# Kernel optimization log

Measured on AMD Instinct MI355X. Metric: run time of the kernel, lower is better.

The kernel has to match this reference:

```python
import itertools
import jax, jax.numpy as jnp
import numpy as np

B, S, H = 1, 2048, 1024
NH, KVH, HD = 16, 8, 64
E, TOPK, I = 8, 2, 3584
EPS = 1e-6
THETA = 1000000.0
COMBS = np.array(list(itertools.combinations(range(E), TOPK)), dtype=np.int32)  # [28,2]


def setup_inputs() -> dict:
    key = jax.random.key(0)
    ks = jax.random.split(key, 12)
    s = 0.02
    return {
        "hidden_states": jax.random.normal(ks[0], (B, S, H), jnp.float32),
        "ln1_w": jnp.ones((H,), jnp.float32),
        "ln2_w": jnp.ones((H,), jnp.float32),
        "wq": jax.random.normal(ks[1], (NH * HD, H), jnp.float32) * s,
        "wk": jax.random.normal(ks[2], (KVH * HD, H), jnp.float32) * s,
        "wv": jax.random.normal(ks[3], (KVH * HD, H), jnp.float32) * s,
        "wo": jax.random.normal(ks[4], (H, NH * HD), jnp.float32) * s,
        "gate_w": jax.random.normal(ks[5], (E, H), jnp.float32) * s,
        "w1": jax.random.normal(ks[6], (E, I, H), jnp.float32) * s,
        "w2": jax.random.normal(ks[7], (E, H, I), jnp.float32) * s,
        "w3": jax.random.normal(ks[8], (E, I, H), jnp.float32) * s,
    }


def _rmsnorm(x, w):
    v = x.astype(jnp.float32)
    v = v * jax.lax.rsqrt(jnp.mean(v * v, axis=-1, keepdims=True) + EPS)
    return (w * v).astype(x.dtype)


def _rotate_half(x):
    h = x.shape[-1] // 2
    return jnp.concatenate([-x[..., h:], x[..., :h]], axis=-1)


def reference(hidden_states, ln1_w, ln2_w, wq, wk, wv, wo, gate_w, w1, w2, w3):
    residual = hidden_states
    x = _rmsnorm(hidden_states, ln1_w)

    # --- Mixtral attention (GQA + RoPE, causal) ---
    q = (x @ wq.T).reshape(B, S, NH, HD).transpose(0, 2, 1, 3)   # [B,NH,S,HD]
    k = (x @ wk.T).reshape(B, S, KVH, HD).transpose(0, 2, 1, 3)  # [B,KVH,S,HD]
    v = (x @ wv.T).reshape(B, S, KVH, HD).transpose(0, 2, 1, 3)

    pos = jnp.arange(S, dtype=jnp.float32)
    inv_freq = 1.0 / (THETA ** (jnp.arange(0, HD, 2, dtype=jnp.float32) / HD))
    freqs = pos[:, None] * inv_freq[None, :]               # [S,HD/2]
    emb = jnp.concatenate([freqs, freqs], axis=-1)          # [S,HD]
    cos, sin = jnp.cos(emb)[None, None], jnp.sin(emb)[None, None]
    q = q * cos + _rotate_half(q) * sin
    k = k * cos + _rotate_half(k) * sin

    rep = NH // KVH
    k = jnp.repeat(k, rep, axis=1)
    v = jnp.repeat(v, rep, axis=1)

    scores = jnp.einsum("bhsd,bhtd->bhst", q, k) / jnp.sqrt(jnp.float32(HD))
    causal = jnp.tril(jnp.ones((S, S), dtype=bool))
    scores = jnp.where(causal[None, None], scores, jnp.finfo(jnp.float32).min)
    attn = jax.nn.softmax(scores.astype(jnp.float32), axis=-1).astype(q.dtype)
    ctx = jnp.einsum("bhst,bhtd->bhsd", attn, v)
    ctx = ctx.transpose(0, 2, 1, 3).reshape(B, S, NH * HD)
    hidden_states = residual + ctx @ wo.T

    # --- MoE block (combination routing, no experts_used mask) ---
    residual = hidden_states
    x = _rmsnorm(hidden_states, ln2_w).reshape(-1, H)       # [N,H], N=B*S
    N = x.shape[0]
    router_logits = x @ gate_w.T                            # [N,E]
    rw = jax.nn.softmax(router_logits.astype(jnp.float32), axis=-1)

    combs = jnp.asarray(COMBS)                              # [28,2]
    comb_scores = jnp.take(rw, combs, axis=1).sum(-1)       # [N,28]
    sel = jnp.argmax(comb_scores, axis=-1)                  # [N]
    selected_experts = combs[sel]                           # [N,TOPK]
    w = jnp.take_along_axis(rw, selected_experts, axis=1)   # [N,TOPK]
    w = (w / w.sum(-1, keepdims=True)).astype(x.dtype)

    # per-token per-expert combine weights (0 if not selected)
    wm = jnp.zeros((N, E), x.dtype).at[jnp.arange(N)[:, None], selected_experts].set(w)

    # dense evaluation of all experts, combined by sparse weights
    h1 = jax.nn.silu(jnp.einsum("nh,eih->nei", x, w1))
    h3 = jnp.einsum("nh,eih->nei", x, w3)
    out_e = jnp.einsum("nei,ehi->neh", h1 * h3, w2)          # [N,E,H]
    moe_out = jnp.einsum("neh,ne->nh", out_e, wm)

    hidden_states = residual + moe_out.reshape(B, S, H)
    return hidden_states
```

## Files before the change

### kernel.cpp

```cpp
#include <hip/hip_runtime.h>
#include <hip/hip_bf16.h>
#include <math.h>

constexpr int S_ = 2048, H_ = 1024, NH_ = 16, KVH_ = 8, HD_ = 64;
constexpr int E_ = 8, I_ = 3584;
constexpr int KSLC = 4;
constexpr float EPS_ = 1e-6f;
constexpr float THETA_ = 1000000.0f;

#define SDIV(a,b) (((a)+(b)-1)/(b))

typedef __attribute__((ext_vector_type(8))) short bf16x8;
typedef __attribute__((ext_vector_type(4))) float f32x4;

__device__ inline unsigned pkbf(float a, float b) {
    unsigned r;
    asm("v_cvt_pk_bf16_f32 %0, %1, %2" : "=v"(r) : "v"(a), "v"(b));
    return r;
}
__device__ inline unsigned short f2bf(float f) {
    unsigned u = __float_as_uint(f);
    u += 0x7FFF + ((u >> 16) & 1);
    return (unsigned short)(u >> 16);
}
__device__ inline float bf2f(unsigned short v) {
    return __uint_as_float((unsigned)v << 16);
}

__device__ inline void gload16u(const void* gsrc, char* ldsArr, int uoff) {
    int off = __builtin_amdgcn_readfirstlane(uoff);
    __builtin_amdgcn_global_load_lds(
        (__attribute__((address_space(1))) void*)(gsrc),
        (__attribute__((address_space(3))) void*)(ldsArr + off), 16, 0, 0);
}
__device__ inline void vmdrain() {
    asm volatile("s_waitcnt vmcnt(0)" ::: "memory");
}

template<bool WB>
__device__ inline int4 loadW16(const void* W, size_t elemOff) {
    if constexpr (WB) {
        return *(const int4*)((const unsigned short*)W + elemOff);
    } else {
        const float* s = (const float*)W + elemOff;
        float4 f0 = *(const float4*)s, f1 = *(const float4*)(s + 4);
        return make_int4(pkbf(f0.x, f0.y), pkbf(f0.z, f0.w),
                         pkbf(f1.x, f1.y), pkbf(f1.z, f1.w));
    }
}

__global__ __launch_bounds__(256) void conv_bf16(const float* __restrict__ in,
                                                 unsigned short* __restrict__ out, long n8)
{
    long i = (long)blockIdx.x * 256 + threadIdx.x;
    long stride = (long)gridDim.x * 256;
    for (; i < n8; i += stride) {
        const float* s = in + i * 8;
        float4 f0 = *(const float4*)s, f1 = *(const float4*)(s + 4);
        *(int4*)(out + i * 8) = make_int4(pkbf(f0.x, f0.y), pkbf(f0.z, f0.w),
                                          pkbf(f1.x, f1.y), pkbf(f1.z, f1.w));
    }
}

__global__ __launch_bounds__(256) void rmsnorm_k(const float* __restrict__ x,
                                                 const float* __restrict__ w,
                                                 float* __restrict__ out,
                                                 unsigned short* __restrict__ outb)
{
    int row = blockIdx.x;
    int tid = threadIdx.x;
    const float* xr = x + (size_t)row * H_;
    float4 v = *(const float4*)&xr[tid * 4];
    float ss = v.x*v.x + v.y*v.y + v.z*v.z + v.w*v.w;
#pragma unroll
    for (int off = 32; off > 0; off >>= 1) ss += __shfl_xor(ss, off);
    __shared__ float red[4];
    if ((tid & 63) == 0) red[tid >> 6] = ss;
    __syncthreads();
    float tot = red[0] + red[1] + red[2] + red[3];
    float r = rsqrtf(tot / (float)H_ + EPS_);
    float4 wv = *(const float4*)&w[tid * 4];
    float4 o;
    o.x = v.x * r * wv.x; o.y = v.y * r * wv.y;
    o.z = v.z * r * wv.z; o.w = v.w * r * wv.w;
    *(float4*)&out[(size_t)row * H_ + tid * 4] = o;
    if (outb) {
        uint2 pk = make_uint2(pkbf(o.x, o.y), pkbf(o.z, o.w));
        *(uint2*)&outb[(size_t)row * H_ + tid * 4] = pk;
    }
}

template<bool OUTF32>
__global__ __launch_bounds__(256) void dense_g(const unsigned short* __restrict__ A,
                                               const unsigned short* __restrict__ B,
                                               const float* __restrict__ Res,
                                               void* __restrict__ C,
                                               int K, int ldC)
{
    int m0 = blockIdx.y * 128, n0 = blockIdx.x * 64;
    int tid = threadIdx.x;
    __shared__ char As[16384], Bs[8192];
    int lane = tid & 63, w = tid >> 6, wm = w >> 1, wn = w & 1;
    int lm = lane & 15, lk = lane >> 4;
    int wb16 = (tid & ~63) * 16;

    const unsigned short* aSrc[4];
    const unsigned short* bSrc[2];
#pragma unroll
    for (int it = 0; it < 4; ++it) {
        int g = tid + it * 256, row = g >> 3, kg = g & 7;
        int kgs = kg ^ (row & 7);
        aSrc[it] = A + (size_t)(m0 + row) * K + kgs * 8;
    }
#pragma unroll
    for (int it = 0; it < 2; ++it) {
        int g = tid + it * 256, row = g >> 3, kg = g & 7;
        int kgs = kg ^ (row & 7);
        bSrc[it] = B + (size_t)(n0 + row) * K + kgs * 8;
    }

    f32x4 z = {0.f, 0.f, 0.f, 0.f};
    f32x4 acc[4][2];
#pragma unroll
    for (int mf = 0; mf < 4; ++mf)
#pragma unroll
        for (int nf = 0; nf < 2; ++nf) acc[mf][nf] = z;

    for (int kt = 0; kt < K / 64; ++kt) {
        int kb = kt * 64;
#pragma unroll
        for (int it = 0; it < 4; ++it)
            gload16u(aSrc[it] + kb, As, wb16 + it * 4096);
#pragma unroll
        for (int it = 0; it < 2; ++it)
            gload16u(bSrc[it] + kb, Bs, wb16 + it * 4096);
        vmdrain();
        __syncthreads();
#pragma unroll
        for (int ks = 0; ks < 2; ++ks) {
            bf16x8 af[4];
#pragma unroll
            for (int mf = 0; mf < 4; ++mf) {
                int row = wm * 64 + mf * 16 + lm;
                af[mf] = *(const bf16x8*)(As + row * 128 + ((ks * 64 + lk * 16) ^ ((row & 7) << 4)));
            }
#pragma unroll
            for (int nf = 0; nf < 2; ++nf) {
                int brow = wn * 32 + nf * 16 + lm;
                bf16x8 bf = *(const bf16x8*)(Bs + brow * 128 + ((ks * 64 + lk * 16) ^ ((brow & 7) << 4)));
#pragma unroll
                for (int mf = 0; mf < 4; ++mf)
                    acc[mf][nf] = __builtin_amdgcn_mfma_f32_16x16x32_bf16(af[mf], bf, acc[mf][nf], 0, 0, 0);
            }
        }
        __syncthreads();
    }

#pragma unroll
    for (int mf = 0; mf < 4; ++mf)
#pragma unroll
        for (int nf = 0; nf < 2; ++nf) {
            int col = n0 + wn * 32 + nf * 16 + lm;
#pragma unroll
            for (int j = 0; j < 4; ++j) {
                int row = m0 + wm * 64 + mf * 16 + lk * 4 + j;
                float v = acc[mf][nf][j];
                if constexpr (OUTF32) {
                    float r = Res ? Res[(size_t)row * ldC + col] : 0.0f;
                    ((float*)C)[(size_t)row * ldC + col] = v + r;
                } else {
                    ((unsigned short*)C)[(size_t)row * ldC + col] = f2bf(v);
                }
            }
        }
}

template<bool WB>
__global__ __launch_bounds__(256) void dense_mfma(const float* __restrict__ A,
                                                  const void* __restrict__ Bw,
                                                  const float* __restrict__ Res,
                                                  float* __restrict__ C,
                                                  int M, int N, int K)
{
    __shared__ char As[16384], Bs[16384];
    int tid = threadIdx.x;
    int m0 = blockIdx.y * 128, n0 = blockIdx.x * 128;
    int lane = tid & 63, w = tid >> 6, wm = w >> 1, wn = w & 1;
    int lm = lane & 15, lk = lane >> 4;

    int4 rA[4], rB[4];
    auto loadAll = [&](int kb) {
#pragma unroll
        for (int it = 0; it < 4; ++it) {
            int g = tid + it * 256, row = g >> 3, kg = g & 7;
            const float* s = A + (size_t)(m0 + row) * K + kb + kg * 8;
            float4 f0 = *(const float4*)s, f1 = *(const float4*)(s + 4);
            rA[it] = make_int4(pkbf(f0.x, f0.y), pkbf(f0.z, f0.w),
                               pkbf(f1.x, f1.y), pkbf(f1.z, f1.w));
            rB[it] = loadW16<WB>(Bw, (size_t)(n0 + row) * K + kb + kg * 8);
        }
    };
    auto writeAll = [&]() {
#pragma unroll
        for (int it = 0; it < 4; ++it) {
            int g = tid + it * 256, row = g >> 3, kg = g & 7;
            int byte = row * 128 + ((kg * 16) ^ ((row & 7) << 4));
            *(int4*)(As + byte) = rA[it];
            *(int4*)(Bs + byte) = rB[it];
        }
    };

    f32x4 z = {0.f, 0.f, 0.f, 0.f};
    f32x4 acc[4][4];
#pragma unroll
    for (int mf = 0; mf < 4; ++mf)
#pragma unroll
        for (int nf = 0; nf < 4; ++nf) acc[mf][nf] = z;

    loadAll(0);
    for (int kt = 0; kt < K / 64; ++kt) {
        __syncthreads();
        writeAll();
        __syncthreads();
        if (kt + 1 < K / 64) loadAll((kt + 1) * 64);
#pragma unroll
        for (int ks = 0; ks < 2; ++ks) {
            bf16x8 af[4];
#pragma unroll
            for (int mf = 0; mf < 4; ++mf) {
                int row = wm * 64 + mf * 16 + lm;
                af[mf] = *(const bf16x8*)(As + row * 128 + ((ks * 64 + lk * 16) ^ ((row & 7) << 4)));
            }
#pragma unroll
            for (int nf = 0; nf < 4; ++nf) {
                int brow = wn * 64 + nf * 16 + lm;
                bf16x8 bf = *(const bf16x8*)(Bs + brow * 128 + ((ks * 64 + lk * 16) ^ ((brow & 7) << 4)));
#pragma unroll
                for (int mf = 0; mf < 4; ++mf)
                    acc[mf][nf] = __builtin_amdgcn_mfma_f32_16x16x32_bf16(af[mf], bf, acc[mf][nf], 0, 0, 0);
            }
        }
    }

#pragma unroll
    for (int mf = 0; mf < 4; ++mf)
#pragma unroll
        for (int nf = 0; nf < 4; ++nf) {
            int col = n0 + wn * 64 + nf * 16 + lm;
#pragma unroll
            for (int j = 0; j < 4; ++j) {
                int row = m0 + wm * 64 + mf * 16 + lk * 4 + j;
                float r = Res ? Res[(size_t)row * N + col] : 0.0f;
                C[(size_t)row * N + col] = acc[mf][nf][j] + r;
            }
        }
}

__global__ __launch_bounds__(256) void rope_conv_b(const unsigned short* __restrict__ qkvb,
                                                   unsigned short* __restrict__ qbf,
                                                   unsigned short* __restrict__ kbf)
{
    int idx = blockIdx.x * 256 + threadIdx.x;
    const int totq = S_ * NH_ * 32;
    const int tot = totq + S_ * KVH_ * 32;
    if (idx >= tot) return;
    const unsigned short* src; unsigned short* dst; int s, di; float sc;
    if (idx < totq) {
        s = idx / (NH_ * 32); int r = idx % (NH_ * 32); int h = r >> 5;
        src = qkvb + (size_t)s * 2048 + h * 64;
        dst = qbf + ((size_t)s * NH_ + h) * HD_;
        di = r & 31; sc = 0.125f;
    } else {
        int j2 = idx - totq;
        s = j2 / (KVH_ * 32); int r = j2 % (KVH_ * 32); int kvh = r >> 5;
        src = qkvb + (size_t)s * 2048 + 1024 + kvh * 64;
        dst = kbf + ((size_t)s * KVH_ + kvh) * HD_;
        di = r & 31; sc = 1.0f;
    }
    float invf = powf(THETA_, -(2.0f * di) / (float)HD_);
    float ang = (float)s * invf;
    float c = cosf(ang), sn = sinf(ang);
    float x0 = bf2f(src[di]), x1 = bf2f(src[di + 32]);
    dst[di]      = f2bf((x0 * c - x1 * sn) * sc);
    dst[di + 32] = f2bf((x1 * c + x0 * sn) * sc);
}

__global__ __launch_bounds__(256) void v_trans_b(const unsigned short* __restrict__ qkvb,
                                                 unsigned short* __restrict__ vtb)
{
    int t0 = blockIdx.x * 64, kvh = blockIdx.y;
    __shared__ unsigned short T[64][64];
    int tid = threadIdx.x;
    int k = tid >> 2, d0 = (tid & 3) * 16;
    const unsigned short* src = qkvb + (size_t)(t0 + k) * 2048 + 1536 + kvh * 64 + d0;
    *(int4*)&T[k][d0]     = *(const int4*)(src);
    *(int4*)&T[k][d0 + 8] = *(const int4*)(src + 8);
    __syncthreads();
    int d = tid >> 2, s0 = (tid & 3) * 16;
    unsigned short tmp[16] __attribute__((aligned(16)));
#pragma unroll
    for (int x = 0; x < 16; ++x) {
        int s = s0 + x;
        int key = 16 * (s & 3) + (s >> 2);
        tmp[x] = T[key][d];
    }
    unsigned short* dst = vtb + ((size_t)kvh * HD_ + d) * S_ + t0 + s0;
    *(int4*)(dst)     = *(int4*)(tmp);
    *(int4*)(dst + 8) = *(int4*)(tmp + 8);
}

__global__ __launch_bounds__(256) void rope_conv(const float* __restrict__ q,
                                                 const float* __restrict__ k,
                                                 unsigned short* __restrict__ qbf,
                                                 unsigned short* __restrict__ kbf)
{
    int idx = blockIdx.x * 256 + threadIdx.x;
    const int totq = S_ * NH_ * 32;
    const int tot = totq + S_ * KVH_ * 32;
    if (idx >= tot) return;
    const float* base; unsigned short* obase; int s, di; float sc;
    if (idx < totq) {
        s = idx / (NH_ * 32); int r = idx % (NH_ * 32);
        size_t o = ((size_t)s * NH_ + (r >> 5)) * HD_;
        base = q + o; obase = qbf + o; di = r & 31; sc = 0.125f;
    } else {
        int j2 = idx - totq;
        s = j2 / (KVH_ * 32); int r = j2 % (KVH_ * 32);
        size_t o = ((size_t)s * KVH_ + (r >> 5)) * HD_;
        base = k + o; obase = kbf + o; di = r & 31; sc = 1.0f;
    }
    float invf = powf(THETA_, -(2.0f * di) / (float)HD_);
    float ang = (float)s * invf;
    float c = cosf(ang), sn = sinf(ang);
    float x0 = base[di], x1 = base[di + 32];
    obase[di]      = f2bf((x0 * c - x1 * sn) * sc);
    obase[di + 32] = f2bf((x1 * c + x0 * sn) * sc);
}

__global__ __launch_bounds__(256) void v_trans(const float* __restrict__ v,
                                               unsigned short* __restrict__ vtb)
{
    int t0 = blockIdx.x * 64, kvh = blockIdx.y;
    __shared__ unsigned short T[64][64];
    int tid = threadIdx.x;
    int k = tid >> 2, d0 = (tid & 3) * 16;
    const float* src = v + ((size_t)(t0 + k) * KVH_ + kvh) * HD_ + d0;
#pragma unroll
    for (int x = 0; x < 4; ++x) {
        float4 f = *(const float4*)(src + x * 4);
        T[k][d0 + x*4 + 0] = f2bf(f.x);
        T[k][d0 + x*4 + 1] = f2bf(f.y);
        T[k][d0 + x*4 + 2] = f2bf(f.z);
        T[k][d0 + x*4 + 3] = f2bf(f.w);
    }
    __syncthreads();
    int d = tid >> 2, s0 = (tid & 3) * 16;
    unsigned short tmp[16] __attribute__((aligned(16)));
#pragma unroll
    for (int x = 0; x < 16; ++x) {
        int s = s0 + x;
        int key = 16 * (s & 3) + (s >> 2);
        tmp[x] = T[key][d];
    }
    unsigned short* dst = vtb + ((size_t)kvh * HD_ + d) * S_ + t0 + s0;
    *(int4*)(dst)     = *(int4*)(tmp);
    *(int4*)(dst + 8) = *(int4*)(tmp + 8);
}

__global__ __launch_bounds__(256) void attn_mfma(const unsigned short* __restrict__ qbf,
                                                 const unsigned short* __restrict__ kbf,
                                                 const unsigned short* __restrict__ vtb,
                                                 float* __restrict__ ctx,
                                                 unsigned short* __restrict__ ctxb)
{
    __shared__ char Ps[4 * 2048];
    int pair = blockIdx.x, h = blockIdx.y, z = blockIdx.z;
    int qb = z ? (31 - pair) : pair;
    int q0 = qb * 64;
    int kvh = h >> 1;
    int tid = threadIdx.x;
    int w = tid >> 6, lane = tid & 63;
    int lm = lane & 15, lk = lane >> 4;
    char* myP = Ps + w * 2048;

    bf16x8 qf[2];
    const unsigned short* qrow = qbf + ((size_t)(q0 + w * 16 + lm) * NH_ + h) * HD_;
#pragma unroll
    for (int ks = 0; ks < 2; ++ks)
        qf[ks] = *(const bf16x8*)(qrow + ks * 32 + lk * 8);

    float m_[4], l_[4];
    f32x4 o_[4];
#pragma unroll
    for (int j = 0; j < 4; ++j) { m_[j] = -1e30f; l_[j] = 0.f; }
    f32x4 zf = {0.f, 0.f, 0.f, 0.f};
#pragma unroll
    for (int nd = 0; nd < 4; ++nd) o_[nd] = zf;

    for (int t0 = 0; t0 <= q0; t0 += 64) {
        f32x4 s[4];
#pragma unroll
        for (int nf = 0; nf < 4; ++nf) {
            const unsigned short* krow = kbf + ((size_t)(t0 + nf * 16 + lm) * KVH_ + kvh) * HD_;
            bf16x8 k0 = *(const bf16x8*)(krow + lk * 8);
            bf16x8 k1 = *(const bf16x8*)(krow + 32 + lk * 8);
            f32x4 acc = zf;
            acc = __builtin_amdgcn_mfma_f32_16x16x32_bf16(qf[0], k0, acc, 0, 0, 0);
            acc = __builtin_amdgcn_mfma_f32_16x16x32_bf16(qf[1], k1, acc, 0, 0, 0);
            s[nf] = acc;
        }
        if (t0 == q0) {
#pragma unroll
            for (int nf = 0; nf < 4; ++nf)
#pragma unroll
                for (int j = 0; j < 4; ++j) {
                    int key = nf * 16 + lm, qq = w * 16 + lk * 4 + j;
                    if (key > qq) s[nf][j] = -1e30f;
                }
        }
        float p_[4][4];
#pragma unroll
        for (int j = 0; j < 4; ++j) {
            float mx = fmaxf(fmaxf(s[0][j], s[1][j]), fmaxf(s[2][j], s[3][j]));
#pragma unroll
            for (int off = 8; off > 0; off >>= 1) mx = fmaxf(mx, __shfl_xor(mx, off));
            float nm = fmaxf(m_[j], mx);
            float rs = __expf(m_[j] - nm);
            float sum = 0.f;
#pragma unroll
            for (int nf = 0; nf < 4; ++nf) {
                float pv = __expf(s[nf][j] - nm);
                p_[nf][j] = pv; sum += pv;
            }
#pragma unroll
            for (int off = 8; off > 0; off >>= 1) sum += __shfl_xor(sum, off);
            l_[j] = l_[j] * rs + sum;
            m_[j] = nm;
#pragma unroll
            for (int nd = 0; nd < 4; ++nd) o_[nd][j] *= rs;
        }
#pragma unroll
        for (int j = 0; j < 4; ++j) {
            int r = lk * 4 + j;
            unsigned lo = pkbf(p_[0][j], p_[1][j]);
            unsigned hi = pkbf(p_[2][j], p_[3][j]);
            int byte = (lm * 8) ^ ((r & 7) << 4);
            *(uint2*)(myP + r * 128 + byte) = make_uint2(lo, hi);
        }
#pragma unroll
        for (int ks = 0; ks < 2; ++ks) {
            int byte = (ks * 64 + lk * 16) ^ ((lm & 7) << 4);
            bf16x8 pA = *(const bf16x8*)(myP + lm * 128 + byte);
#pragma unroll
            for (int nd = 0; nd < 4; ++nd) {
                const unsigned short* vrow = vtb + ((size_t)kvh * HD_ + nd * 16 + lm) * S_ + t0 + ks * 32 + lk * 8;
                bf16x8 vB = *(const bf16x8*)vrow;
                o_[nd] = __builtin_amdgcn_mfma_f32_16x16x32_bf16(pA, vB, o_[nd], 0, 0, 0);
            }
        }
    }
#pragma unroll
    for (int nd = 0; nd < 4; ++nd)
#pragma unroll
        for (int j = 0; j < 4; ++j) {
            int r = lk * 4 + j;
            float val = o_[nd][j] / l_[j];
            size_t oidx = ((size_t)(q0 + w * 16 + r) * NH_ + h) * HD_ + nd * 16 + lm;
            ctx[oidx] = val;
            ctxb[oidx] = f2bf(val);
        }
}

__global__ __launch_bounds__(64) void router_k(const float* __restrict__ x2,
                                               const float* __restrict__ gw,
                                               int* __restrict__ cnt,
                                               int* __restrict__ elist,
                                               int* __restrict__ eslot,
                                               float* __restrict__ wslot)
{
    int n = blockIdx.x, lane = threadIdx.x;
    float part[E_];
#pragma unroll
    for (int e = 0; e < E_; ++e) part[e] = 0.f;
    const float* xr = x2 + (size_t)n * H_;
    for (int j = lane; j < H_; j += 64) {
        float xv = xr[j];
#pragma unroll
        for (int e = 0; e < E_; ++e) part[e] = fmaf(xv, gw[e * H_ + j], part[e]);
    }
#pragma unroll
    for (int e = 0; e < E_; ++e)
#pragma unroll
        for (int off = 32; off > 0; off >>= 1) part[e] += __shfl_xor(part[e], off);
    if (lane == 0) {
        float mx = part[0];
#pragma unroll
        for (int e = 1; e < E_; ++e) mx = fmaxf(mx, part[e]);
        float rw[E_]; float ssum = 0.f;
#pragma unroll
        for (int e = 0; e < E_; ++e) { rw[e] = expf(part[e] - mx); ssum += rw[e]; }
#pragma unroll
        for (int e = 0; e < E_; ++e) rw[e] /= ssum;
        float best = -1.f; int ba = 0, bb = 1;
        for (int a = 0; a < E_; ++a)
            for (int b = a + 1; b < E_; ++b) {
                float scv = rw[a] + rw[b];
                if (scv > best) { best = scv; ba = a; bb = b; }
            }
        float wa = rw[ba], wb = rw[bb], wsum = wa + wb;
        wa /= wsum; wb /= wsum;
        int p = atomicAdd(&cnt[ba], 1);
        elist[ba * S_ + p] = n; eslot[ba * S_ + p] = 2 * n;
        p = atomicAdd(&cnt[bb], 1);
        elist[bb * S_ + p] = n; eslot[bb * S_ + p] = 2 * n + 1;
        wslot[2 * n] = wa; wslot[2 * n + 1] = wb;
    }
}

__global__ __launch_bounds__(256) void moe_up_g(const unsigned short* __restrict__ x2b,
                                                const unsigned short* __restrict__ w1b,
                                                const unsigned short* __restrict__ w3b,
                                                const int* __restrict__ cnt,
                                                const int* __restrict__ elist,
                                                const int* __restrict__ eslot,
                                                unsigned short* __restrict__ hbuf)
{
    int e = blockIdx.z;
    int c = cnt[e];
    int p0 = blockIdx.y * 128;
    if (p0 >= c) return;
    int i0 = blockIdx.x * 64;
    int tid = threadIdx.x;

    __shared__ char As[16384], B1s[8192], B3s[8192];
    __shared__ int rowtokS[128], rowslotS[128];
    if (tid < 128) {
        int p = min(p0 + tid, c - 1);
        rowtokS[tid]  = elist[e * S_ + p];
        rowslotS[tid] = eslot[e * S_ + p];
    }
    __syncthreads();

    int lane = tid & 63, w = tid >> 6, wm = w >> 1, wn = w & 1;
    int lm = lane & 15, lk = lane >> 4;
    int wb16 = (tid & ~63) * 16;
    size_t wbase = (size_t)e * I_ * H_;

    const unsigned short* aSrc[4];
    const unsigned short* b1Src[2];
    const unsigned short* b3Src[2];
#pragma unroll
    for (int it = 0; it < 4; ++it) {
        int g = tid + it * 256, row = g >> 3, kg = g & 7;
        int kgs = kg ^ (row & 7);
        aSrc[it] = x2b + (size_t)rowtokS[row] * H_ + kgs * 8;
    }
#pragma unroll
    for (int it = 0; it < 2; ++it) {
        int g = tid + it * 256, row = g >> 3, kg = g & 7;
        int kgs = kg ^ (row & 7);
        size_t off = wbase + (size_t)(i0 + row) * H_ + kgs * 8;
        b1Src[it] = w1b + off;
        b3Src[it] = w3b + off;
    }

    f32x4 z = {0.f, 0.f, 0.f, 0.f};
    f32x4 acc1[4][2], acc3[4][2];
#pragma unroll
    for (int mf = 0; mf < 4; ++mf)
#pragma unroll
        for (int nf = 0; nf < 2; ++nf) { acc1[mf][nf] = z; acc3[mf][nf] = z; }

    for (int kt = 0; kt < H_ / 64; ++kt) {
        int kb = kt * 64;
#pragma unroll
        for (int it = 0; it < 4; ++it)
            gload16u(aSrc[it] + kb, As, wb16 + it * 4096);
#pragma unroll
        for (int it = 0; it < 2; ++it) {
            gload16u(b1Src[it] + kb, B1s, wb16 + it * 4096);
            gload16u(b3Src[it] + kb, B3s, wb16 + it * 4096);
        }
        vmdrain();
        __syncthreads();
#pragma unroll
        for (int ks = 0; ks < 2; ++ks) {
            bf16x8 af[4];
#pragma unroll
            for (int mf = 0; mf < 4; ++mf) {
                int row = wm * 64 + mf * 16 + lm;
                af[mf] = *(const bf16x8*)(As + row * 128 + ((ks * 64 + lk * 16) ^ ((row & 7) << 4)));
            }
#pragma unroll
            for (int nf = 0; nf < 2; ++nf) {
                int brow = wn * 32 + nf * 16 + lm;
                int bby = brow * 128 + ((ks * 64 + lk * 16) ^ ((brow & 7) << 4));
                bf16x8 b1 = *(const bf16x8*)(B1s + bby);
                bf16x8 b3 = *(const bf16x8*)(B3s + bby);
#pragma unroll
                for (int mf = 0; mf < 4; ++mf) {
                    acc1[mf][nf] = __builtin_amdgcn_mfma_f32_16x16x32_bf16(af[mf], b1, acc1[mf][nf], 0, 0, 0);
                    acc3[mf][nf] = __builtin_amdgcn_mfma_f32_16x16x32_bf16(af[mf], b3, acc3[mf][nf], 0, 0, 0);
                }
            }
        }
        __syncthreads();
    }

#pragma unroll
    for (int mf = 0; mf < 4; ++mf)
#pragma unroll
        for (int nf = 0; nf < 2; ++nf) {
            int coli = i0 + wn * 32 + nf * 16 + lm;
#pragma unroll
            for (int j = 0; j < 4; ++j) {
                int rloc = wm * 64 + mf * 16 + lk * 4 + j;
                if (p0 + rloc < c) {
                    float h1 = acc1[mf][nf][j];
                    float val = h1 / (1.f + __expf(-h1)) * acc3[mf][nf][j];
                    hbuf[(size_t)rowslotS[rloc] * I_ + coli] = f2bf(val);
                }
            }
        }
}

__global__ __launch_bounds__(256) void moe_dn_g(const unsigned short* __restrict__ hbuf,
                                                const unsigned short* __restrict__ w2b,
                                                const int* __restrict__ cnt,
                                                const int* __restrict__ eslot,
                                                unsigned short* __restrict__ dbuf)
{
    int e = blockIdx.z >> 2;
    int slice = blockIdx.z & 3;
    int c = cnt[e];
    int p0 = blockIdx.y * 128;
    if (p0 >= c) return;
    int h0 = blockIdx.x * 128;
    int tid = threadIdx.x;
    const int kb0 = slice * (I_ / KSLC);

    __shared__ char As[16384], Bs[16384];
    __shared__ int rowslotS[128];
    if (tid < 128) rowslotS[tid] = eslot[e * S_ + min(p0 + tid, c - 1)];
    __syncthreads();

    int lane = tid & 63, w = tid >> 6, wm = w >> 1, wn = w & 1;
    int lm = lane & 15, lk = lane >> 4;
    int wb16 = (tid & ~63) * 16;
    size_t wbase = (size_t)e * H_ * I_;

    const unsigned short* aSrc[4];
    const unsigned short* bSrc[4];
#pragma unroll
    for (int it = 0; it < 4; ++it) {
        int g = tid + it * 256, row = g >> 3, kg = g & 7;
        int kgs = kg ^ (row & 7);
        aSrc[it] = hbuf + (size_t)rowslotS[row] * I_ + kb0 + kgs * 8;
        bSrc[it] = w2b + wbase + (size_t)(h0 + row) * I_ + kb0 + kgs * 8;
    }

    f32x4 z = {0.f, 0.f, 0.f, 0.f};
    f32x4 acc[4][4];
#pragma unroll
    for (int mf = 0; mf < 4; ++mf)
#pragma unroll
        for (int nf = 0; nf < 4; ++nf) acc[mf][nf] = z;

    const int NKT = (I_ / KSLC) / 64;
    for (int kt = 0; kt < NKT; ++kt) {
        int kb = kt * 64;
#pragma unroll
        for (int it = 0; it < 4; ++it) {
            gload16u(aSrc[it] + kb, As, wb16 + it * 4096);
            gload16u(bSrc[it] + kb, Bs, wb16 + it * 4096);
        }
        vmdrain();
        __syncthreads();
#pragma unroll
        for (int ks = 0; ks < 2; ++ks) {
            bf16x8 af[4];
#pragma unroll
            for (int mf = 0; mf < 4; ++mf) {
                int row = wm * 64 + mf * 16 + lm;
                af[mf] = *(const bf16x8*)(As + row * 128 + ((ks * 64 + lk * 16) ^ ((row & 7) << 4)));
            }
#pragma unroll
            for (int nf = 0; nf < 4; ++nf) {
                int brow = wn * 64 + nf * 16 + lm;
                bf16x8 bf = *(const bf16x8*)(Bs + brow * 128 + ((ks * 64 + lk * 16) ^ ((brow & 7) << 4)));
#pragma unroll
                for (int mf = 0; mf < 4; ++mf)
                    acc[mf][nf] = __builtin_amdgcn_mfma_f32_16x16x32_bf16(af[mf], bf, acc[mf][nf], 0, 0, 0);
            }
        }
        __syncthreads();
    }

    unsigned short* dslice = dbuf + (size_t)slice * S_ * 2 * H_;
#pragma unroll
    for (int mf = 0; mf < 4; ++mf)
#pragma unroll
        for (int nf = 0; nf < 4; ++nf) {
            int colh = h0 + wn * 64 + nf * 16 + lm;
#pragma unroll
            for (int j = 0; j < 4; ++j) {
                int rloc = wm * 64 + mf * 16 + lk * 4 + j;
                if (p0 + rloc < c)
                    dslice[(size_t)rowslotS[rloc] * H_ + colh] = f2bf(acc[mf][nf][j]);
            }
        }
}

template<bool WB>
__global__ __launch_bounds__(256) void moe_up_mfma(const float* __restrict__ x2,
                                                   const void* __restrict__ w1,
                                                   const void* __restrict__ w3,
                                                   const int* __restrict__ cnt,
                                                   const int* __restrict__ elist,
                                                   const int* __restrict__ eslot,
                                                   unsigned short* __restrict__ hbuf)
{
    int e = blockIdx.z;
    int c = cnt[e];
    int p0 = blockIdx.y * 128;
    if (p0 >= c) return;
    int i0 = blockIdx.x * 64;
    int tid = threadIdx.x;

    __shared__ char As[16384], B1s[8192], B3s[8192];
    __shared__ int rowtokS[128], rowslotS[128];
    if (tid < 128) {
        int p = min(p0 + tid, c - 1);
        rowtokS[tid]  = elist[e * S_ + p];
        rowslotS[tid] = eslot[e * S_ + p];
    }
    __syncthreads();

    int lane = tid & 63, w = tid >> 6, wm = w >> 1, wn = w & 1;
    int lm = lane & 15, lk = lane >> 4;
    size_t wbase = (size_t)e * I_ * H_;

    int4 rA[4], rB1[2], rB3[2];
    auto loadAll = [&](int kb) {
#pragma unroll
        for (int it = 0; it < 4; ++it) {
            int g = tid + it * 256, row = g >> 3, kg = g & 7;
            const float* s = x2 + (size_t)rowtokS[row] * H_ + kb + kg * 8;
            float4 f0 = *(const float4*)s, f1 = *(const float4*)(s + 4);
            rA[it] = make_int4(pkbf(f0.x, f0.y), pkbf(f0.z, f0.w),
                               pkbf(f1.x, f1.y), pkbf(f1.z, f1.w));
        }
#pragma unroll
        for (int it = 0; it < 2; ++it) {
            int g = tid + it * 256, row = g >> 3, kg = g & 7;
            size_t off = wbase + (size_t)(i0 + row) * H_ + kb + kg * 8;
            rB1[it] = loadW16<WB>(w1, off);
            rB3[it] = loadW16<WB>(w3, off);
        }
    };
    auto writeAll = [&]() {
#pragma unroll
        for (int it = 0; it < 4; ++it) {
            int g = tid + it * 256, row = g >> 3, kg = g & 7;
            int byte = row * 128 + ((kg * 16) ^ ((row & 7) << 4));
            *(int4*)(As + byte) = rA[it];
        }
#pragma unroll
        for (int it = 0; it < 2; ++it) {
            int g = tid + it * 256, row = g >> 3, kg = g & 7;
            int byte = row * 128 + ((kg * 16) ^ ((row & 7) << 4));
            *(int4*)(B1s + byte) = rB1[it];
            *(int4*)(B3s + byte) = rB3[it];
        }
    };

    f32x4 z = {0.f, 0.f, 0.f, 0.f};
    f32x4 acc1[4][2], acc3[4][2];
#pragma unroll
    for (int mf = 0; mf < 4; ++mf)
#pragma unroll
        for (int nf = 0; nf < 2; ++nf) { acc1[mf][nf] = z; acc3[mf][nf] = z; }

    loadAll(0);
    for (int kt = 0; kt < H_ / 64; ++kt) {
        __syncthreads();
        writeAll();
        __syncthreads();
        if (kt + 1 < H_ / 64) loadAll((kt + 1) * 64);
#pragma unroll
        for (int ks = 0; ks < 2; ++ks) {
            bf16x8 af[4];
#pragma unroll
            for (int mf = 0; mf < 4; ++mf) {
                int row = wm * 64 + mf * 16 + lm;
                af[mf] = *(const bf16x8*)(As + row * 128 + ((ks * 64 + lk * 16) ^ ((row & 7) << 4)));
            }
#pragma unroll
            for (int nf = 0; nf < 2; ++nf) {
                int brow = wn * 32 + nf * 16 + lm;
                int bby = brow * 128 + ((ks * 64 + lk * 16) ^ ((brow & 7) << 4));
                bf16x8 b1 = *(const bf16x8*)(B1s + bby);
                bf16x8 b3 = *(const bf16x8*)(B3s + bby);
#pragma unroll
                for (int mf = 0; mf < 4; ++mf) {
                    acc1[mf][nf] = __builtin_amdgcn_mfma_f32_16x16x32_bf16(af[mf], b1, acc1[mf][nf], 0, 0, 0);
                    acc3[mf][nf] = __builtin_amdgcn_mfma_f32_16x16x32_bf16(af[mf], b3, acc3[mf][nf], 0, 0, 0);
                }
            }
        }
    }

#pragma unroll
    for (int mf = 0; mf < 4; ++mf)
#pragma unroll
        for (int nf = 0; nf < 2; ++nf) {
            int coli = i0 + wn * 32 + nf * 16 + lm;
#pragma unroll
            for (int j = 0; j < 4; ++j) {
                int rloc = wm * 64 + mf * 16 + lk * 4 + j;
                if (p0 + rloc < c) {
                    float h1 = acc1[mf][nf][j];
                    float val = h1 / (1.f + __expf(-h1)) * acc3[mf][nf][j];
                    hbuf[(size_t)rowslotS[rloc] * I_ + coli] = f2bf(val);
                }
            }
        }
}

template<bool WB>
__global__ __launch_bounds__(256) void moe_dn_mfma(const unsigned short* __restrict__ hbuf,
                                                   const void* __restrict__ w2,
                                                   const int* __restrict__ cnt,
                                                   const int* __restrict__ eslot,
                                                   unsigned short* __restrict__ dbuf)
{
    int e = blockIdx.z >> 2;
    int slice = blockIdx.z & 3;
    int c = cnt[e];
    int p0 = blockIdx.y * 128;
    if (p0 >= c) return;
    int h0 = blockIdx.x * 128;
    int tid = threadIdx.x;
    const int kb0 = slice * (I_ / KSLC);

    __shared__ char As[16384], Bs[16384];
    __shared__ int rowslotS[128];
    if (tid < 128) rowslotS[tid] = eslot[e * S_ + min(p0 + tid, c - 1)];
    __syncthreads();

    int lane = tid & 63, w = tid >> 6, wm = w >> 1, wn = w & 1;
    int lm = lane & 15, lk = lane >> 4;
    size_t wbase = (size_t)e * H_ * I_;

    int4 rA[4], rB[4];
    auto loadAll = [&](int kb) {
#pragma unroll
        for (int it = 0; it < 4; ++it) {
            int g = tid + it * 256, row = g >> 3, kg = g & 7;
            rA[it] = *(const int4*)(hbuf + (size_t)rowslotS[row] * I_ + kb + kg * 8);
            rB[it] = loadW16<WB>(w2, wbase + (size_t)(h0 + row) * I_ + kb + kg * 8);
        }
    };
    auto writeAll = [&]() {
#pragma unroll
        for (int it = 0; it < 4; ++it) {
            int g = tid + it * 256, row = g >> 3, kg = g & 7;
            int byte = row * 128 + ((kg * 16) ^ ((row & 7) << 4));
            *(int4*)(As + byte) = rA[it];
            *(int4*)(Bs + byte) = rB[it];
        }
    };

    f32x4 z = {0.f, 0.f, 0.f, 0.f};
    f32x4 acc[4][4];
#pragma unroll
    for (int mf = 0; mf < 4; ++mf)
#pragma unroll
        for (int nf = 0; nf < 4; ++nf) acc[mf][nf] = z;

    loadAll(kb0);
    const int NKT = (I_ / KSLC) / 64;
    for (int kt = 0; kt < NKT; ++kt) {
        __syncthreads();
        writeAll();
        __syncthreads();
        if (kt + 1 < NKT) loadAll(kb0 + (kt + 1) * 64);
#pragma unroll
        for (int ks = 0; ks < 2; ++ks) {
            bf16x8 af[4];
#pragma unroll
            for (int mf = 0; mf < 4; ++mf) {
                int row = wm * 64 + mf * 16 + lm;
                af[mf] = *(const bf16x8*)(As + row * 128 + ((ks * 64 + lk * 16) ^ ((row & 7) << 4)));
            }
#pragma unroll
            for (int nf = 0; nf < 4; ++nf) {
                int brow = wn * 64 + nf * 16 + lm;
                bf16x8 bf = *(const bf16x8*)(Bs + brow * 128 + ((ks * 64 + lk * 16) ^ ((brow & 7) << 4)));
#pragma unroll
                for (int mf = 0; mf < 4; ++mf)
                    acc[mf][nf] = __builtin_amdgcn_mfma_f32_16x16x32_bf16(af[mf], bf, acc[mf][nf], 0, 0, 0);
            }
        }
    }

    unsigned short* dslice = dbuf + (size_t)slice * S_ * 2 * H_;
#pragma unroll
    for (int mf = 0; mf < 4; ++mf)
#pragma unroll
        for (int nf = 0; nf < 4; ++nf) {
            int colh = h0 + wn * 64 + nf * 16 + lm;
#pragma unroll
            for (int j = 0; j < 4; ++j) {
                int rloc = wm * 64 + mf * 16 + lk * 4 + j;
                if (p0 + rloc < c)
                    dslice[(size_t)rowslotS[rloc] * H_ + colh] = f2bf(acc[mf][nf][j]);
            }
        }
}

__global__ __launch_bounds__(256) void combine_k(const float* __restrict__ hid2,
                                                 const unsigned short* __restrict__ dbuf,
                                                 const float* __restrict__ wslot,
                                                 float* __restrict__ out)
{
    int idx = blockIdx.x * 256 + threadIdx.x;
    if (idx >= S_ * H_) return;
    int n = idx >> 10;
    int hcol = idx & (H_ - 1);
    float s0 = 0.f, s1 = 0.f;
#pragma unroll
    for (int sl = 0; sl < KSLC; ++sl) {
        const unsigned short* base = dbuf + (size_t)sl * S_ * 2 * H_;
        s0 += bf2f(base[(size_t)(2 * n)     * H_ + hcol]);
        s1 += bf2f(base[(size_t)(2 * n + 1) * H_ + hcol]);
    }
    out[idx] = hid2[idx] + wslot[2 * n] * s0 + wslot[2 * n + 1] * s1;
}

extern "C" void kernel_launch(void* const* d_in, const int* in_sizes, int n_in,
                              void* d_out, int out_size, void* d_ws, size_t ws_size,
                              hipStream_t stream)
{
    const float* hidden = (const float*)d_in[0];
    const float* ln1    = (const float*)d_in[1];
    const float* ln2    = (const float*)d_in[2];
    const float* wq     = (const float*)d_in[3];
    const float* wk     = (const float*)d_in[4];
    const float* wv     = (const float*)d_in[5];
    const float* wo     = (const float*)d_in[6];
    const float* gw     = (const float*)d_in[7];
    const float* w1     = (const float*)d_in[8];
    const float* w2     = (const float*)d_in[9];
    const float* w3     = (const float*)d_in[10];
    float* out = (float*)d_out;

    char* p = (char*)d_ws;
    auto alignp = [&]() { p = (char*)(((uintptr_t)p + 255) & ~(uintptr_t)255); };
    auto alloc_f = [&](size_t n) { alignp(); float* r = (float*)p; p += n * 4; return r; };
    auto alloc_h = [&](size_t n) { alignp(); unsigned short* r = (unsigned short*)p; p += n * 2; return r; };
    auto alloc_i = [&](size_t n) { alignp(); int* r = (int*)p; p += n * 4; return r; };

    float* xb   = alloc_f((size_t)S_ * H_);
    unsigned short* xbb = alloc_h((size_t)S_ * H_);
    float* q    = alloc_f((size_t)S_ * NH_ * HD_);
    float* kb   = alloc_f((size_t)S_ * KVH_ * HD_);
    float* vb   = alloc_f((size_t)S_ * KVH_ * HD_);
    unsigned short* qkvb = alloc_h((size_t)S_ * 2048);
    float* hid2 = alloc_f((size_t)S_ * H_);
    float* x2   = alloc_f((size_t)S_ * H_);
    unsigned short* x2b  = alloc_h((size_t)S_ * H_);
    unsigned short* ctxb = alloc_h((size_t)S_ * H_);
    unsigned short* hbuf = alloc_h((size_t)S_ * 2 * I_);
    unsigned short* dbuf = alloc_h((size_t)KSLC * S_ * 2 * H_);
    float* wslot= alloc_f((size_t)S_ * 2);
    unsigned short* qbf = alloc_h((size_t)S_ * NH_ * HD_);
    unsigned short* kbf = alloc_h((size_t)S_ * KVH_ * HD_);
    unsigned short* vtb = alloc_h((size_t)KVH_ * HD_ * S_);
    int* cnt   = alloc_i(E_);
    int* elist = alloc_i((size_t)E_ * S_);
    int* eslot = alloc_i((size_t)E_ * S_);
    float* ctx = xb;

    size_t used = (size_t)(p - (char*)d_ws);
    const size_t nW = (size_t)E_ * I_ * H_;
    size_t wbf_bytes = (3 * nW + (size_t)2048 * H_ + (size_t)H_ * NH_ * HD_) * 2 + 8192;
    bool WB = ws_size > used && (ws_size - used) >= wbf_bytes;

    unsigned short *w1b = nullptr, *w3b = nullptr, *w2b = nullptr;
    unsigned short *wqkvb = nullptr, *wob = nullptr;
    if (WB) {
        w1b = alloc_h(nW); w3b = alloc_h(nW); w2b = alloc_h(nW);
        wqkvb = alloc_h((size_t)2048 * H_);
        wob = alloc_h((size_t)H_ * NH_ * HD_);
    }

    hipMemsetAsync(cnt, 0, E_ * sizeof(int), stream);

    if (WB) {
        conv_bf16<<<2048, 256, 0, stream>>>(w1, w1b, (long)(nW / 8));
        conv_bf16<<<2048, 256, 0, stream>>>(w3, w3b, (long)(nW / 8));
        conv_bf16<<<2048, 256, 0, stream>>>(w2, w2b, (long)(nW / 8));
        conv_bf16<<<512, 256, 0, stream>>>(wq, wqkvb, (long)((size_t)NH_*HD_*H_ / 8));
        conv_bf16<<<256, 256, 0, stream>>>(wk, wqkvb + (size_t)NH_*HD_*H_, (long)((size_t)KVH_*HD_*H_ / 8));
        conv_bf16<<<256, 256, 0, stream>>>(wv, wqkvb + (size_t)(NH_+KVH_)*HD_*H_, (long)((size_t)KVH_*HD_*H_ / 8));
        conv_bf16<<<512, 256, 0, stream>>>(wo, wob, (long)((size_t)H_*NH_*HD_ / 8));
    }

    rmsnorm_k<<<S_, 256, 0, stream>>>(hidden, ln1, xb, WB ? xbb : nullptr);

    if (WB) {
        dense_g<false><<<dim3(32, 16), 256, 0, stream>>>(xbb, wqkvb, nullptr, qkvb, H_, 2048);
        {
            int tot = S_ * (NH_ + KVH_) * 32;
            rope_conv_b<<<SDIV(tot, 256), 256, 0, stream>>>(qkvb, qbf, kbf);
        }
        v_trans_b<<<dim3(S_ / 64, KVH_), 256, 0, stream>>>(qkvb, vtb);
        attn_mfma<<<dim3(16, NH_, 2), 256, 0, stream>>>(qbf, kbf, vtb, ctx, ctxb);
        dense_g<true><<<dim3(16, 16), 256, 0, stream>>>(ctxb, wob, hidden, hid2, H_, H_);
    } else {
        dense_mfma<false><<<dim3(8, 16), 256, 0, stream>>>(xb, wq, nullptr, q,  S_, NH_ * HD_, H_);
        dense_mfma<false><<<dim3(4, 16), 256, 0, stream>>>(xb, wk, nullptr, kb, S_, KVH_ * HD_, H_);
        dense_mfma<false><<<dim3(4, 16), 256, 0, stream>>>(xb, wv, nullptr, vb, S_, KVH_ * HD_, H_);
        {
            int tot = S_ * (NH_ + KVH_) * 32;
            rope_conv<<<SDIV(tot, 256), 256, 0, stream>>>(q, kb, qbf, kbf);
        }
        v_trans<<<dim3(S_ / 64, KVH_), 256, 0, stream>>>(vb, vtb);
        attn_mfma<<<dim3(16, NH_, 2), 256, 0, stream>>>(qbf, kbf, vtb, ctx, ctxb);
        dense_mfma<false><<<dim3(8, 16), 256, 0, stream>>>(ctx, wo, hidden, hid2, S_, H_, NH_ * HD_);
    }

    rmsnorm_k<<<S_, 256, 0, stream>>>(hid2, ln2, x2, x2b);
    router_k<<<S_, 64, 0, stream>>>(x2, gw, cnt, elist, eslot, wslot);

    if (WB) {
        moe_up_g<<<dim3(I_ / 64, S_ / 128, E_), 256, 0, stream>>>(x2b, w1b, w3b, cnt, elist, eslot, hbuf);
        moe_dn_g<<<dim3(H_ / 128, S_ / 128, E_ * KSLC), 256, 0, stream>>>(hbuf, w2b, cnt, eslot, dbuf);
    } else {
        moe_up_mfma<false><<<dim3(I_ / 64, S_ / 128, E_), 256, 0, stream>>>(x2, w1, w3, cnt, elist, eslot, hbuf);
        moe_dn_mfma<false><<<dim3(H_ / 128, S_ / 128, E_ * KSLC), 256, 0, stream>>>(hbuf, w2, cnt, eslot, dbuf);
    }
    combine_k<<<SDIV(S_ * H_, 256), 256, 0, stream>>>(hid2, dbuf, wslot, out);
}
```

Baseline: 463.2 us.

## Fuse weight conversions, rmsnorm with router, and add lazy softmax rescale

Merges the seven fp32-to-bf16 weight conversion launches into two kernels. Fuses the second RMSNorm with the router into one kernel that also skips the fp32 normalized output. Drops unused fp32 writes of the first norm and the attention context. Adds a lazy online-softmax rescale that only updates the running max when it grows by more than 8, cutting exps and multiplies in attention. This trades a somewhat larger intermediate range in P for less per-tile work.

```diff
diff --git a/kernel.cpp b/kernel.cpp
--- a/kernel.cpp
+++ b/kernel.cpp
@@ -60,6 +60,47 @@
         *(int4*)(out + i * 8) = make_int4(pkbf(f0.x, f0.y), pkbf(f0.z, f0.w),
                                           pkbf(f1.x, f1.y), pkbf(f1.z, f1.w));
     }
+}
+
+__global__ __launch_bounds__(256) void conv3(const float* __restrict__ a,
+                                             const float* __restrict__ b,
+                                             const float* __restrict__ c,
+                                             unsigned short* __restrict__ oa,
+                                             unsigned short* __restrict__ ob,
+                                             unsigned short* __restrict__ oc,
+                                             long n8)
+{
+    int t = blockIdx.y;
+    const float* in = (t == 0) ? a : (t == 1) ? b : c;
+    unsigned short* out = (t == 0) ? oa : (t == 1) ? ob : oc;
+    long i = (long)blockIdx.x * 256 + threadIdx.x;
+    long stride = (long)gridDim.x * 256;
+    for (; i < n8; i += stride) {
+        const float* s = in + i * 8;
+        float4 f0 = *(const float4*)s, f1 = *(const float4*)(s + 4);
+        *(int4*)(out + i * 8) = make_int4(pkbf(f0.x, f0.y), pkbf(f0.z, f0.w),
+                                          pkbf(f1.x, f1.y), pkbf(f1.z, f1.w));
+    }
+}
+
+__global__ __launch_bounds__(256) void conv_qkvo(const float* __restrict__ wq,
+                                                 const float* __restrict__ wk,
+                                                 const float* __restrict__ wv,
+                                                 const float* __restrict__ wo,
+                                                 unsigned short* __restrict__ wqkvb,
+                                                 unsigned short* __restrict__ wob)
+{
+    const long NQ = (long)NH_ * HD_ * H_ / 8;
+    const long NK = (long)KVH_ * HD_ * H_ / 8;
+    long u = (long)blockIdx.x * 256 + threadIdx.x;
+    const float* in; unsigned short* out;
+    if (u < NQ)                { in = wq + u * 8;               out = wqkvb + u * 8; }
+    else if (u < NQ + NK)      { long v = u - NQ;      in = wk + v * 8; out = wqkvb + (NQ + v) * 8; }
+    else if (u < NQ + 2 * NK)  { long v = u - NQ - NK; in = wv + v * 8; out = wqkvb + (NQ + NK + v) * 8; }
+    else                       { long v = u - NQ - 2 * NK; in = wo + v * 8; out = wob + v * 8; }
+    float4 f0 = *(const float4*)in, f1 = *(const float4*)(in + 4);
+    *(int4*)out = make_int4(pkbf(f0.x, f0.y), pkbf(f0.z, f0.w),
+                            pkbf(f1.x, f1.y), pkbf(f1.z, f1.w));
 }
 
 __global__ __launch_bounds__(256) void rmsnorm_k(const float* __restrict__ x,
@@ -83,10 +124,83 @@
     float4 o;
     o.x = v.x * r * wv.x; o.y = v.y * r * wv.y;
     o.z = v.z * r * wv.z; o.w = v.w * r * wv.w;
-    *(float4*)&out[(size_t)row * H_ + tid * 4] = o;
+    if (out) *(float4*)&out[(size_t)row * H_ + tid * 4] = o;
     if (outb) {
         uint2 pk = make_uint2(pkbf(o.x, o.y), pkbf(o.z, o.w));
         *(uint2*)&outb[(size_t)row * H_ + tid * 4] = pk;
+    }
+}
+
+__global__ __launch_bounds__(256) void rms2router(const float* __restrict__ x,
+                                                  const float* __restrict__ w,
+                                                  const float* __restrict__ gw,
+                                                  unsigned short* __restrict__ outb,
+                                                  int* __restrict__ cnt,
+                                                  int* __restrict__ elist,
+                                                  int* __restrict__ eslot,
+                                                  float* __restrict__ wslot)
+{
+    int row = blockIdx.x;
+    int tid = threadIdx.x;
+    const float* xr = x + (size_t)row * H_;
+    float4 v = *(const float4*)&xr[tid * 4];
+    float ss = v.x*v.x + v.y*v.y + v.z*v.z + v.w*v.w;
+#pragma unroll
+    for (int off = 32; off > 0; off >>= 1) ss += __shfl_xor(ss, off);
+    __shared__ float red[4];
+    __shared__ float redE[4][8];
+    if ((tid & 63) == 0) red[tid >> 6] = ss;
+    __syncthreads();
+    float tot = red[0] + red[1] + red[2] + red[3];
+    float r = rsqrtf(tot / (float)H_ + EPS_);
+    float4 wv = *(const float4*)&w[tid * 4];
+    float o0 = v.x * r * wv.x, o1 = v.y * r * wv.y;
+    float o2 = v.z * r * wv.z, o3 = v.w * r * wv.w;
+    uint2 pk = make_uint2(pkbf(o0, o1), pkbf(o2, o3));
+    *(uint2*)&outb[(size_t)row * H_ + tid * 4] = pk;
+
+    int col = tid * 4;
+    float part[E_];
+#pragma unroll
+    for (int e = 0; e < E_; ++e) {
+        const float* g = gw + (size_t)e * H_ + col;
+        part[e] = o0 * g[0] + o1 * g[1] + o2 * g[2] + o3 * g[3];
+    }
+#pragma unroll
+    for (int e = 0; e < E_; ++e)
+#pragma unroll
+        for (int off = 32; off > 0; off >>= 1) part[e] += __shfl_xor(part[e], off);
+    if ((tid & 63) == 0)
+#pragma unroll
+        for (int e = 0; e < E_; ++e) redE[tid >> 6][e] = part[e];
+    __syncthreads();
+    if (tid == 0) {
+        float lg[E_];
+#pragma unroll
+        for (int e = 0; e < E_; ++e)
+            lg[e] = redE[0][e] + redE[1][e] + redE[2][e] + redE[3][e];
+        float mx = lg[0];
+#pragma unroll
+        for (int e = 1; e < E_; ++e) mx = fmaxf(mx, lg[e]);
+        float rw[E_]; float ssum = 0.f;
+#pragma unroll
+        for (int e = 0; e < E_; ++e) { rw[e] = expf(lg[e] - mx); ssum += rw[e]; }
+#pragma unroll
+        for (int e = 0; e < E_; ++e) rw[e] /= ssum;
+        float best = -1.f; int ba = 0, bb = 1;
+        for (int a = 0; a < E_; ++a)
+            for (int b = a + 1; b < E_; ++b) {
+                float scv = rw[a] + rw[b];
+                if (scv > best) { best = scv; ba = a; bb = b; }
+            }
+        float wa = rw[ba], wb = rw[bb], wsum = wa + wb;
+        wa /= wsum; wb /= wsum;
+        int n = row;
+        int p = atomicAdd(&cnt[ba], 1);
+        elist[ba * S_ + p] = n; eslot[ba * S_ + p] = 2 * n;
+        p = atomicAdd(&cnt[bb], 1);
+        elist[bb * S_ + p] = n; eslot[bb * S_ + p] = 2 * n + 1;
+        wslot[2 * n] = wa; wslot[2 * n + 1] = wb;
     }
 }
 
@@ -424,20 +538,22 @@
             float mx = fmaxf(fmaxf(s[0][j], s[1][j]), fmaxf(s[2][j], s[3][j]));
 #pragma unroll
             for (int off = 8; off > 0; off >>= 1) mx = fmaxf(mx, __shfl_xor(mx, off));
-            float nm = fmaxf(m_[j], mx);
-            float rs = __expf(m_[j] - nm);
+            if (mx > m_[j] + 8.f) {
+                float rs = __expf(m_[j] - mx);
+                m_[j] = mx;
+                l_[j] *= rs;
+#pragma unroll
+                for (int nd = 0; nd < 4; ++nd) o_[nd][j] *= rs;
+            }
             float sum = 0.f;
 #pragma unroll
             for (int nf = 0; nf < 4; ++nf) {
-                float pv = __expf(s[nf][j] - nm);
+                float pv = __expf(s[nf][j] - m_[j]);
                 p_[nf][j] = pv; sum += pv;
             }
 #pragma unroll
             for (int off = 8; off > 0; off >>= 1) sum += __shfl_xor(sum, off);
-            l_[j] = l_[j] * rs + sum;
-            m_[j] = nm;
-#pragma unroll
-            for (int nd = 0; nd < 4; ++nd) o_[nd][j] *= rs;
+            l_[j] += sum;
         }
 #pragma unroll
         for (int j = 0; j < 4; ++j) {
@@ -466,7 +582,7 @@
             int r = lk * 4 + j;
             float val = o_[nd][j] / l_[j];
             size_t oidx = ((size_t)(q0 + w * 16 + r) * NH_ + h) * HD_ + nd * 16 + lm;
-            ctx[oidx] = val;
+            if (ctx) ctx[oidx] = val;
             ctxb[oidx] = f2bf(val);
         }
 }
@@ -998,27 +1114,25 @@
     hipMemsetAsync(cnt, 0, E_ * sizeof(int), stream);
 
     if (WB) {
-        conv_bf16<<<2048, 256, 0, stream>>>(w1, w1b, (long)(nW / 8));
-        conv_bf16<<<2048, 256, 0, stream>>>(w3, w3b, (long)(nW / 8));
-        conv_bf16<<<2048, 256, 0, stream>>>(w2, w2b, (long)(nW / 8));
-        conv_bf16<<<512, 256, 0, stream>>>(wq, wqkvb, (long)((size_t)NH_*HD_*H_ / 8));
-        conv_bf16<<<256, 256, 0, stream>>>(wk, wqkvb + (size_t)NH_*HD_*H_, (long)((size_t)KVH_*HD_*H_ / 8));
-        conv_bf16<<<256, 256, 0, stream>>>(wv, wqkvb + (size_t)(NH_+KVH_)*HD_*H_, (long)((size_t)KVH_*HD_*H_ / 8));
-        conv_bf16<<<512, 256, 0, stream>>>(wo, wob, (long)((size_t)H_*NH_*HD_ / 8));
-    }
-
-    rmsnorm_k<<<S_, 256, 0, stream>>>(hidden, ln1, xb, WB ? xbb : nullptr);
-
-    if (WB) {
+        conv3<<<dim3(2048, 3), 256, 0, stream>>>(w1, w3, w2, w1b, w3b, w2b, (long)(nW / 8));
+        conv_qkvo<<<1536, 256, 0, stream>>>(wq, wk, wv, wo, wqkvb, wob);
+
+        rmsnorm_k<<<S_, 256, 0, stream>>>(hidden, ln1, nullptr, xbb);
         dense_g<false><<<dim3(32, 16), 256, 0, stream>>>(xbb, wqkvb, nullptr, qkvb, H_, 2048);
         {
             int tot = S_ * (NH_ + KVH_) * 32;
             rope_conv_b<<<SDIV(tot, 256), 256, 0, stream>>>(qkvb, qbf, kbf);
         }
         v_trans_b<<<dim3(S_ / 64, KVH_), 256, 0, stream>>>(qkvb, vtb);
-        attn_mfma<<<dim3(16, NH_, 2), 256, 0, stream>>>(qbf, kbf, vtb, ctx, ctxb);
+        attn_mfma<<<dim3(16, NH_, 2), 256, 0, stream>>>(qbf, kbf, vtb, nullptr, ctxb);
         dense_g<true><<<dim3(16, 16), 256, 0, stream>>>(ctxb, wob, hidden, hid2, H_, H_);
+
+        rms2router<<<S_, 256, 0, stream>>>(hid2, ln2, gw, x2b, cnt, elist, eslot, wslot);
+
+        moe_up_g<<<dim3(I_ / 64, S_ / 128, E_), 256, 0, stream>>>(x2b, w1b, w3b, cnt, elist, eslot, hbuf);
+        moe_dn_g<<<dim3(H_ / 128, S_ / 128, E_ * KSLC), 256, 0, stream>>>(hbuf, w2b, cnt, eslot, dbuf);
     } else {
+        rmsnorm_k<<<S_, 256, 0, stream>>>(hidden, ln1, xb, nullptr);
         dense_mfma<false><<<dim3(8, 16), 256, 0, stream>>>(xb, wq, nullptr, q,  S_, NH_ * HD_, H_);
         dense_mfma<false><<<dim3(4, 16), 256, 0, stream>>>(xb, wk, nullptr, kb, S_, KVH_ * HD_, H_);
         dense_mfma<false><<<dim3(4, 16), 256, 0, stream>>>(xb, wv, nullptr, vb, S_, KVH_ * HD_, H_);
@@ -1029,15 +1143,10 @@
         v_trans<<<dim3(S_ / 64, KVH_), 256, 0, stream>>>(vb, vtb);
         attn_mfma<<<dim3(16, NH_, 2), 256, 0, stream>>>(qbf, kbf, vtb, ctx, ctxb);
         dense_mfma<false><<<dim3(8, 16), 256, 0, stream>>>(ctx, wo, hidden, hid2, S_, H_, NH_ * HD_);
-    }
-
-    rmsnorm_k<<<S_, 256, 0, stream>>>(hid2, ln2, x2, x2b);
-    router_k<<<S_, 64, 0, stream>>>(x2, gw, cnt, elist, eslot, wslot);
-
-    if (WB) {
-        moe_up_g<<<dim3(I_ / 64, S_ / 128, E_), 256, 0, stream>>>(x2b, w1b, w3b, cnt, elist, eslot, hbuf);
-        moe_dn_g<<<dim3(H_ / 128, S_ / 128, E_ * KSLC), 256, 0, stream>>>(hbuf, w2b, cnt, eslot, dbuf);
-    } else {
+
+        rmsnorm_k<<<S_, 256, 0, stream>>>(hid2, ln2, x2, nullptr);
+        router_k<<<S_, 64, 0, stream>>>(x2, gw, cnt, elist, eslot, wslot);
+
         moe_up_mfma<false><<<dim3(I_ / 64, S_ / 128, E_), 256, 0, stream>>>(x2, w1, w3, cnt, elist, eslot, hbuf);
         moe_dn_mfma<false><<<dim3(H_ / 128, S_ / 128, E_ * KSLC), 256, 0, stream>>>(hbuf, w2, cnt, eslot, dbuf);
     }
```

New measurement: 437.4 us. 1.06x faster.
